# Optimization experiments

Hardware: AMD Instinct MI355X
Metric: run time of the kernel (lower is better)

## Reference

```python
import jax, jax.numpy as jnp
import numpy as np

CODEBOOK = 512


def setup_inputs() -> dict:
    key = jax.random.key(0)
    k1, k2 = jax.random.split(key)
    h = jax.random.normal(k1, (8, 128, 32, 32), dtype=jnp.float32)
    emb = jax.random.normal(k2, (CODEBOOK, 1), dtype=jnp.float32)
    return {"h": h, "emb": emb}


def reference(h, emb):
    # Scalar VQ: map each element of h to its nearest codebook entry
    # (embedding dim is 1, so distance is just |e - x|).
    flat = h.reshape(-1)                      # [N]
    codes = emb[:, 0]                         # [K]
    dist = jnp.abs(flat[:, None] - codes[None, :])   # [N, K]
    idx = jnp.argmin(dist, axis=1)            # [N]
    return codes[idx].reshape(h.shape)
```

## Files before the change

kernel.cpp:

```cpp
#include <hip/hip_runtime.h>

#define NCODE 512
#define NB    2048
#define NTHR  1024
#define FINF  __builtin_huge_valf()

__device__ __forceinline__ unsigned int fmap(float f) {
    unsigned int b = __float_as_uint(f);
    return b ^ ((b & 0x80000000u) ? 0xFFFFFFFFu : 0x80000000u);
}
__device__ __forceinline__ float funmap(unsigned int u) {
    unsigned int b = (u & 0x80000000u) ? (u ^ 0x80000000u) : ~u;
    return __uint_as_float(b);
}
__device__ __forceinline__ int bucket_of(float x, float vmin, float invw) {
    float bf = fminf(fmaxf((x - vmin) * invw, 0.0f), (float)(NB - 1));
    return (int)bf;
}
__device__ __forceinline__ bool pick_hi(float x, float vl, float vh,
                                        unsigned int il, unsigned int ih) {
    float dl = x - vl;
    float dh = vh - x;
    return (dh < dl) || ((dh == dl) && (ih < il));
}

__global__ __launch_bounds__(NTHR) void quantize_fused(
        const float* __restrict__ emb,
        const float4* __restrict__ h4,
        float4* __restrict__ out4,
        int n4) {
    __shared__ float4 s_lut[NB];
    __shared__ unsigned int s_excl[NB + 1];
    __shared__ unsigned long long s_tmp[NCODE];
    __shared__ float s_val[NCODE + 16];
    __shared__ float s_thr[NCODE];
    __shared__ unsigned short s_idx[NCODE];
    __shared__ float s_red[32];
    __shared__ unsigned int s_wt[16];

    const int t = threadIdx.x;
    const int lane = t & 63;
    const int wv = t >> 6;

    const int gid = blockIdx.x * NTHR + t;
    const bool live = (gid < n4);
    float4 x4 = make_float4(0.f, 0.f, 0.f, 0.f);
    if (live) x4 = h4[gid];

    s_excl[t] = 0; s_excl[t + NTHR] = 0;
    if (t == 0) s_excl[NB] = 0;

    float v = 0.0f;
    if (t < NCODE) {
        v = emb[t];
        float mn = v, mx = v;
        #pragma unroll
        for (int o = 32; o >= 1; o >>= 1) {
            mn = fminf(mn, __shfl_xor(mn, o));
            mx = fmaxf(mx, __shfl_xor(mx, o));
        }
        if (lane == 0) { s_red[wv] = mn; s_red[16 + wv] = mx; }
    }
    __syncthreads();

    float vmin, invw;
    {
        float m0 = s_red[0], M0 = s_red[16];
        #pragma unroll
        for (int i = 1; i < 8; ++i) { m0 = fminf(m0, s_red[i]); M0 = fmaxf(M0, s_red[16 + i]); }
        vmin = m0;
        float range = M0 - m0;
        invw = (range > 0.0f) ? ((float)NB / range) : 0.0f;
    }

    int b = 0; unsigned int slot = 0;
    unsigned long long myk = 0;
    if (t < NCODE) {
        myk = (((unsigned long long)fmap(v)) << 16) | (unsigned int)t;
        b = bucket_of(v, vmin, invw);
        slot = atomicAdd(&s_excl[b], 1u);
    }
    __syncthreads();

    {
        unsigned int h0 = s_excl[2 * t], h1 = s_excl[2 * t + 1];
        unsigned int s = h0 + h1, incl = s;
        #pragma unroll
        for (int o = 1; o < 64; o <<= 1) {
            unsigned int w = __shfl_up(incl, o);
            if (lane >= o) incl += w;
        }
        if (lane == 63) s_wt[wv] = incl;
        __syncthreads();
        unsigned int base = 0;
        #pragma unroll
        for (int i = 0; i < 16; ++i) base += (i < wv) ? s_wt[i] : 0u;
        unsigned int c0 = base + incl - s;
        s_excl[2 * t] = c0; s_excl[2 * t + 1] = c0 + h0;
        if (t == NTHR - 1) s_excl[NB] = c0 + h0 + h1;
    }
    __syncthreads();

    unsigned int lo_b = 0, hi_b = 0;
    if (t < NCODE) {
        lo_b = s_excl[b]; hi_b = s_excl[b + 1];
        s_tmp[lo_b + slot] = myk;
    }
    __syncthreads();

    if (t < NCODE) {
        int r = 0; unsigned int minEq = (unsigned int)t;
        for (unsigned int j = lo_b; j < hi_b; ++j) {
            unsigned long long k2 = s_tmp[j];
            r += (k2 < myk) ? 1 : 0;
            float v2 = funmap((unsigned int)(k2 >> 16));
            if (v2 == v) {
                unsigned int i2 = (unsigned int)(k2 & 0xFFFFull);
                minEq = (i2 < minEq) ? i2 : minEq;
            }
        }
        int pos = (int)lo_b + r;
        s_val[pos] = v;
        s_idx[pos] = (unsigned short)minEq;
    } else if (t < NCODE + 16) {
        s_val[t] = FINF;
    }
    __syncthreads();

    float thrReg = FINF;
    if (t < NCODE - 1) {
        float vl = s_val[t], vh = s_val[t + 1];
        unsigned int il = s_idx[t], ih = s_idx[t + 1];
        if (vl == vh) {
            thrReg = vl;
        } else {
            unsigned int ulo = fmap(vl), uhi = fmap(vh);
            unsigned int um = fmap(0.5f * (vl + vh));
            unsigned int a  = (um - ulo >= 8u) ? um - 8u : ulo;
            unsigned int b2 = (uhi - um >= 8u) ? um + 8u : uhi;
            if (!pick_hi(funmap(a),  vl, vh, il, ih)) ulo = a;
            if ( pick_hi(funmap(b2), vl, vh, il, ih)) uhi = b2;
            while (uhi - ulo > 1u) {
                unsigned int mid = ulo + ((uhi - ulo) >> 1);
                if (pick_hi(funmap(mid), vl, vh, il, ih)) uhi = mid; else ulo = mid;
            }
            thrReg = funmap(uhi);
        }
        s_thr[t] = thrReg;
    } else if (t == NCODE - 1) {
        s_thr[t] = FINF;
    } else {
        int t2 = t - NCODE;
        s_excl[t2] = 0; s_excl[t2 + 512] = 0; s_excl[t2 + 1024] = 0; s_excl[t2 + 1536] = 0;
        if (t2 == 0) s_excl[NB] = 0;
    }
    __syncthreads();

    if (t < NCODE - 1) atomicAdd(&s_excl[bucket_of(thrReg, vmin, invw)], 1u);
    __syncthreads();

    {
        unsigned int h0 = s_excl[2 * t], h1 = s_excl[2 * t + 1];
        unsigned int s = h0 + h1, incl = s;
        #pragma unroll
        for (int o = 1; o < 64; o <<= 1) {
            unsigned int w = __shfl_up(incl, o);
            if (lane >= o) incl += w;
        }
        if (lane == 63) s_wt[wv] = incl;
        __syncthreads();
        unsigned int base = 0;
        #pragma unroll
        for (int i = 0; i < 16; ++i) base += (i < wv) ? s_wt[i] : 0u;
        unsigned int c0 = base + incl - s;
        s_excl[2 * t] = c0; s_excl[2 * t + 1] = c0 + h0;
        if (t == NTHR - 1) s_excl[NB] = c0 + h0 + h1;
    }
    __syncthreads();

    #pragma unroll
    for (int k = 0; k < 2; ++k) {
        int bb = 2 * t + k;
        unsigned int j = s_excl[bb];
        unsigned int cnt = s_excl[bb + 1] - j;
        float4 w;
        if (cnt <= 3u) {
            w.x = (cnt >= 1u) ? s_thr[j]     : FINF;
            w.y = (cnt >= 2u) ? s_thr[j + 1] : FINF;
            w.z = (cnt >= 3u) ? s_thr[j + 2] : FINF;
            w.w = __uint_as_float(j);
        } else {
            w.x = FINF; w.y = FINF; w.z = FINF;
            w.w = __uint_as_float(j | 0x80000000u);
        }
        s_lut[bb] = w;
    }
    __syncthreads();

    if (live) {
        float xs[4] = {x4.x, x4.y, x4.z, x4.w};
        float rr[4];
        #pragma unroll
        for (int e = 0; e < 4; ++e) {
            float x = xs[e];
            float4 L = s_lut[bucket_of(x, vmin, invw)];
            unsigned int bits = __float_as_uint(L.w);
            int r = (int)(bits & 0xFFFFu);
            r += (x >= L.x) ? 1 : 0;
            r += (x >= L.y) ? 1 : 0;
            r += (x >= L.z) ? 1 : 0;
            if (bits & 0x80000000u) {
                r = 0;
                #pragma unroll
                for (int st = 256; st >= 1; st >>= 1)
                    r += (s_thr[r + st - 1] <= x) ? st : 0;
            }
            rr[e] = s_val[r];
        }
        out4[gid] = make_float4(rr[0], rr[1], rr[2], rr[3]);
    }
}

extern "C" void kernel_launch(void* const* d_in, const int* in_sizes, int n_in,
                              void* d_out, int out_size, void* d_ws, size_t ws_size,
                              hipStream_t stream) {
    const float* h   = (const float*)d_in[0];
    const float* emb = (const float*)d_in[1];
    float* out = (float*)d_out;

    const int n = in_sizes[0];
    const int n4 = n / 4;
    const int blocks = (n4 + NTHR - 1) / NTHR;
    quantize_fused<<<blocks, NTHR, 0, stream>>>(
        emb, (const float4*)h, (float4*)out, n4);
}
```

Baseline: 11.72 us.

## Build bucket LUT via binary search and store code values directly in LUT

Replaces the second histogram, atomics and prefix-scan pass over threshold buckets with a per-bucket binary search over the sorted thresholds, which removes several barriers and a block-wide scan. The LUT entries now hold the answer value directly for buckets with zero or one threshold, so most lookups skip a dependent s_val read. Buckets with two thresholds still read s_val, and buckets with three or more fall back to a full binary search, where the old code used the LUT for up to three. Each block still builds the whole LUT redundantly, and each of its bins now costs a 9-step search.

```diff
diff --git a/kernel.cpp b/kernel.cpp
--- a/kernel.cpp
+++ b/kernel.cpp
@@ -14,13 +14,11 @@
     return __uint_as_float(b);
 }
 __device__ __forceinline__ int bucket_of(float x, float vmin, float invw) {
-    float bf = fminf(fmaxf((x - vmin) * invw, 0.0f), (float)(NB - 1));
-    return (int)bf;
+    return (int)fminf(fmaxf((x - vmin) * invw, 0.0f), (float)(NB - 1));
 }
 __device__ __forceinline__ bool pick_hi(float x, float vl, float vh,
                                         unsigned int il, unsigned int ih) {
-    float dl = x - vl;
-    float dh = vh - x;
+    float dl = x - vl, dh = vh - x;
     return (dh < dl) || ((dh == dl) && (ih < il));
 }
 
@@ -32,9 +30,10 @@
     __shared__ float4 s_lut[NB];
     __shared__ unsigned int s_excl[NB + 1];
     __shared__ unsigned long long s_tmp[NCODE];
-    __shared__ float s_val[NCODE + 16];
+    __shared__ float s_val[NCODE + 4];
     __shared__ float s_thr[NCODE];
     __shared__ unsigned short s_idx[NCODE];
+    __shared__ unsigned short s_j[NB + 1];
     __shared__ float s_red[32];
     __shared__ unsigned int s_wt[16];
 
@@ -49,7 +48,6 @@
 
     s_excl[t] = 0; s_excl[t + NTHR] = 0;
     if (t == 0) s_excl[NB] = 0;
-
     float v = 0.0f;
     if (t < NCODE) {
         v = emb[t];
@@ -73,8 +71,7 @@
         invw = (range > 0.0f) ? ((float)NB / range) : 0.0f;
     }
 
-    int b = 0; unsigned int slot = 0;
-    unsigned long long myk = 0;
+    unsigned long long myk = 0; int b = 0; unsigned int slot = 0;
     if (t < NCODE) {
         myk = (((unsigned long long)fmap(v)) << 16) | (unsigned int)t;
         b = bucket_of(v, vmin, invw);
@@ -84,7 +81,7 @@
 
     {
         unsigned int h0 = s_excl[2 * t], h1 = s_excl[2 * t + 1];
-        unsigned int s = h0 + h1, incl = s;
+        unsigned int ssum = h0 + h1, incl = ssum;
         #pragma unroll
         for (int o = 1; o < 64; o <<= 1) {
             unsigned int w = __shfl_up(incl, o);
@@ -95,7 +92,7 @@
         unsigned int base = 0;
         #pragma unroll
         for (int i = 0; i < 16; ++i) base += (i < wv) ? s_wt[i] : 0u;
-        unsigned int c0 = base + incl - s;
+        unsigned int c0 = base + incl - ssum;
         s_excl[2 * t] = c0; s_excl[2 * t + 1] = c0 + h0;
         if (t == NTHR - 1) s_excl[NB] = c0 + h0 + h1;
     }
@@ -122,15 +119,15 @@
         int pos = (int)lo_b + r;
         s_val[pos] = v;
         s_idx[pos] = (unsigned short)minEq;
-    } else if (t < NCODE + 16) {
-        s_val[t] = FINF;
-    }
-    __syncthreads();
-
-    float thrReg = FINF;
+    } else if (t < NCODE + 4) {
+        s_val[t] = 0.0f;
+    }
+    __syncthreads();
+
     if (t < NCODE - 1) {
         float vl = s_val[t], vh = s_val[t + 1];
         unsigned int il = s_idx[t], ih = s_idx[t + 1];
+        float thrReg;
         if (vl == vh) {
             thrReg = vl;
         } else {
@@ -149,51 +146,47 @@
         s_thr[t] = thrReg;
     } else if (t == NCODE - 1) {
         s_thr[t] = FINF;
-    } else {
-        int t2 = t - NCODE;
-        s_excl[t2] = 0; s_excl[t2 + 512] = 0; s_excl[t2 + 1024] = 0; s_excl[t2 + 1536] = 0;
-        if (t2 == 0) s_excl[NB] = 0;
-    }
-    __syncthreads();
-
-    if (t < NCODE - 1) atomicAdd(&s_excl[bucket_of(thrReg, vmin, invw)], 1u);
-    __syncthreads();
-
-    {
-        unsigned int h0 = s_excl[2 * t], h1 = s_excl[2 * t + 1];
-        unsigned int s = h0 + h1, incl = s;
-        #pragma unroll
-        for (int o = 1; o < 64; o <<= 1) {
-            unsigned int w = __shfl_up(incl, o);
-            if (lane >= o) incl += w;
-        }
-        if (lane == 63) s_wt[wv] = incl;
-        __syncthreads();
-        unsigned int base = 0;
-        #pragma unroll
-        for (int i = 0; i < 16; ++i) base += (i < wv) ? s_wt[i] : 0u;
-        unsigned int c0 = base + incl - s;
-        s_excl[2 * t] = c0; s_excl[2 * t + 1] = c0 + h0;
-        if (t == NTHR - 1) s_excl[NB] = c0 + h0 + h1;
-    }
-    __syncthreads();
-
-    #pragma unroll
-    for (int k = 0; k < 2; ++k) {
-        int bb = 2 * t + k;
-        unsigned int j = s_excl[bb];
-        unsigned int cnt = s_excl[bb + 1] - j;
-        float4 w;
-        if (cnt <= 3u) {
-            w.x = (cnt >= 1u) ? s_thr[j]     : FINF;
-            w.y = (cnt >= 2u) ? s_thr[j + 1] : FINF;
-            w.z = (cnt >= 3u) ? s_thr[j + 2] : FINF;
-            w.w = __uint_as_float(j);
-        } else {
-            w.x = FINF; w.y = FINF; w.z = FINF;
-            w.w = __uint_as_float(j | 0x80000000u);
-        }
-        s_lut[bb] = w;
+    }
+    __syncthreads();
+
+    {
+        #pragma unroll
+        for (int k = 0; k < 2; ++k) {
+            int bb = t + k * NTHR;
+            int r = 0;
+            #pragma unroll
+            for (int st = 256; st >= 1; st >>= 1) {
+                float tv = s_thr[r + st - 1];
+                r += (bucket_of(tv, vmin, invw) < bb) ? st : 0;
+            }
+            s_j[bb] = (unsigned short)r;
+        }
+        if (t == 0) s_j[NB] = (unsigned short)NCODE;
+    }
+    __syncthreads();
+
+    {
+        #pragma unroll
+        for (int k = 0; k < 2; ++k) {
+            int bb = t + k * NTHR;
+            int j0 = s_j[bb], j1 = s_j[bb + 1];
+            int cnt = j1 - j0;
+            float4 L;
+            if (cnt == 0) {
+                L = make_float4(s_val[j0], 0.f, 0.f,
+                                __uint_as_float((unsigned)j0));
+            } else if (cnt == 1) {
+                L = make_float4(s_val[j0], s_thr[j0], s_val[j0 + 1],
+                                __uint_as_float((unsigned)j0 | (1u << 12)));
+            } else if (cnt == 2) {
+                L = make_float4(s_thr[j0], s_thr[j0 + 1], 0.f,
+                                __uint_as_float((unsigned)j0 | (2u << 12)));
+            } else {
+                L = make_float4(0.f, 0.f, 0.f,
+                                __uint_as_float(3u << 12));
+            }
+            s_lut[bb] = L;
+        }
     }
     __syncthreads();
 
@@ -205,17 +198,21 @@
             float x = xs[e];
             float4 L = s_lut[bucket_of(x, vmin, invw)];
             unsigned int bits = __float_as_uint(L.w);
-            int r = (int)(bits & 0xFFFFu);
-            r += (x >= L.x) ? 1 : 0;
-            r += (x >= L.y) ? 1 : 0;
-            r += (x >= L.z) ? 1 : 0;
-            if (bits & 0x80000000u) {
-                r = 0;
-                #pragma unroll
-                for (int st = 256; st >= 1; st >>= 1)
-                    r += (s_thr[r + st - 1] <= x) ? st : 0;
-            }
-            rr[e] = s_val[r];
+            unsigned int c = bits >> 12;
+            float ans = (c == 1 && x >= L.y) ? L.z : L.x;
+            if (c >= 2) {
+                int r;
+                if (c == 3) {
+                    r = 0;
+                    #pragma unroll
+                    for (int st = 256; st >= 1; st >>= 1)
+                        r += (s_thr[r + st - 1] <= x) ? st : 0;
+                } else {
+                    r = (int)(bits & 0xFFFu) + ((x >= L.x) ? 1 : 0) + ((x >= L.y) ? 1 : 0);
+                }
+                ans = s_val[r];
+            }
+            rr[e] = ans;
         }
         out4[gid] = make_float4(rr[0], rr[1], rr[2], rr[3]);
     }
```

Result: slower. 13.14 us (+12.1%).
